# Kernel optimization log

Measured on AMD Instinct MI355X. Metric: run time of the kernel, lower is better.

Reference implementation:

```python
import jax, jax.numpy as jnp
import numpy as np

E = 1024   # embd_size
H = 16     # head_count
HS = E // H
B = 8
T = 1024   # seq len == input_size
EPS = 1e-5

def _ln(x, g, b):
    m = jnp.mean(x, axis=-1, keepdims=True)
    v = jnp.mean((x - m) ** 2, axis=-1, keepdims=True)
    return (x - m) * jax.lax.rsqrt(v + EPS) * g + b

def setup_inputs() -> dict:
    key = jax.random.key(0)
    ks = jax.random.split(key, 12)
    s_attn = 1.0 / np.sqrt(E)
    s_ff1 = 1.0 / np.sqrt(E)
    s_ff2 = 1.0 / np.sqrt(4 * E)
    return {
        "x": jax.random.normal(ks[0], (B, T, E), dtype=jnp.float32),
        "wq": jax.random.normal(ks[1], (H, E, HS), dtype=jnp.float32) * s_attn,
        "wk": jax.random.normal(ks[2], (H, E, HS), dtype=jnp.float32) * s_attn,
        "wv": jax.random.normal(ks[3], (H, E, HS), dtype=jnp.float32) * s_attn,
        "w_proj": jax.random.normal(ks[4], (E, E), dtype=jnp.float32) * s_attn,
        "b_proj": jnp.zeros((E,), dtype=jnp.float32),
        "w1": jax.random.normal(ks[5], (E, 4 * E), dtype=jnp.float32) * s_ff1,
        "b1": jnp.zeros((4 * E,), dtype=jnp.float32),
        "w2": jax.random.normal(ks[6], (4 * E, E), dtype=jnp.float32) * s_ff2,
        "b2": jnp.zeros((E,), dtype=jnp.float32),
        "g1": jnp.ones((E,), dtype=jnp.float32),
        "be1": jnp.zeros((E,), dtype=jnp.float32),
        "g2": jnp.ones((E,), dtype=jnp.float32),
        "be2": jnp.zeros((E,), dtype=jnp.float32),
    }

def reference(x, wq, wk, wv, w_proj, b_proj, w1, b1, w2, b2, g1, be1, g2, be2):
    Tn = x.shape[1]
    h = _ln(x, g1, be1)
    # per-head projections, batched over heads: [B,T,E] x [H,E,S] -> [B,H,T,S]
    q = jnp.einsum('bte,hes->bhts', h, wq)
    k = jnp.einsum('bte,hes->bhts', h, wk)
    v = jnp.einsum('bte,hes->bhts', h, wv)
    scores = jnp.einsum('bhts,bhus->bhtu', q, k)
    # NOTE: source multiplies by sqrt(T) (x.shape[2] of scores), not 1/sqrt(head_size)
    scores = scores * jnp.float32(Tn) ** 0.5
    causal = jnp.tril(jnp.ones((Tn, Tn), dtype=bool))
    scores = jnp.where(causal, scores, -jnp.inf)
    attn = jax.nn.softmax(scores, axis=-1)
    out = jnp.einsum('bhtu,bhus->bhts', attn, v)           # [B,H,T,S]
    out = out.transpose(0, 2, 1, 3).reshape(x.shape[0], Tn, E)  # concat heads
    out = out @ w_proj + b_proj
    x = x + out
    f = _ln(x, g2, be2)
    f = jax.nn.relu(f @ w1 + b1) @ w2 + b2
    return x + f
```

## Files before the change

kernel.cpp:

```cpp
#include <hip/hip_runtime.h>


typedef unsigned short u16;
typedef __attribute__((ext_vector_type(8))) short  bfx8;
typedef __attribute__((ext_vector_type(4))) float  f32x4;
typedef __attribute__((ext_vector_type(4))) unsigned short u16v4;

#define MFMA16 __builtin_amdgcn_mfma_f32_16x16x32_bf16

__device__ __forceinline__ u16 f2bf(float f) {
    union { float f; unsigned u; } c; c.f = f;
    unsigned r = c.u + 0x7fffu + ((c.u >> 16) & 1u);
    return (u16)(r >> 16);
}
__device__ __forceinline__ float bf2f(u16 b) {
    union { unsigned u; float f; } c; c.u = ((unsigned)b) << 16; return c.f;
}
__device__ __forceinline__ float exp2_fast(float x) {
    float r; asm("v_exp_f32 %0, %1" : "=v"(r) : "v"(x)); return r;
}

__device__ __forceinline__ void gl_lds16(const void* g, void* l) {
    void* gg = (void*)g;
    __builtin_amdgcn_global_load_lds(
        (__attribute__((address_space(1))) void*)gg,
        (__attribute__((address_space(3))) void*)l,
        16, 0, 0);
}

__global__ __launch_bounds__(256)
void transpose_split(const float* __restrict__ src, u16* __restrict__ dhi,
                     u16* __restrict__ dlo, int C, int OS,
                     size_t inBS, size_t outBS)
{
    __shared__ float t[64][65];
    const int tid = threadIdx.x;
    const float* s = src + (size_t)blockIdx.z * inBS
                   + ((size_t)blockIdx.y * 64) * C + (size_t)blockIdx.x * 64;
    const size_t obase = (size_t)blockIdx.z * outBS
                       + ((size_t)blockIdx.x * 64) * OS + (size_t)blockIdx.y * 64;
    {
        const int r = tid >> 2, c4 = (tid & 3) * 16;
#pragma unroll
        for (int k = 0; k < 4; ++k) {
            float4 f = *(const float4*)(s + (size_t)r * C + c4 + k * 4);
            t[r][c4 + k*4 + 0] = f.x; t[r][c4 + k*4 + 1] = f.y;
            t[r][c4 + k*4 + 2] = f.z; t[r][c4 + k*4 + 3] = f.w;
        }
    }
    __syncthreads();
    {
        const int c = tid >> 2, r4 = (tid & 3) * 16;
        bfx8 h0, h1, l0, l1;
#pragma unroll
        for (int k = 0; k < 8; ++k) {
            float v0 = t[r4 + k][c];
            float v1 = t[r4 + 8 + k][c];
            u16 a = f2bf(v0), b = f2bf(v1);
            h0[k] = (short)a; h1[k] = (short)b;
            l0[k] = (short)f2bf(v0 - bf2f(a));
            l1[k] = (short)f2bf(v1 - bf2f(b));
        }
        u16* d = dhi + obase + (size_t)c * OS + r4;
        *(bfx8*)d = h0; *(bfx8*)(d + 8) = h1;
        if (dlo) {
            u16* d2 = dlo + obase + (size_t)c * OS + r4;
            *(bfx8*)d2 = l0; *(bfx8*)(d2 + 8) = l1;
        }
    }
}

__global__ __launch_bounds__(256)
void transpose_v(const u16* __restrict__ v, u16* __restrict__ vT)
{
    const int ut = blockIdx.x, h = blockIdx.y, b = blockIdx.z;
    __shared__ u16 t[64][72];
    const int tid = threadIdx.x;
    {
        const int u = tid >> 2, s4 = (tid & 3) * 16;
        const u16* src = v + ((size_t)(b * 1024 + ut * 64 + u)) * 1024 + h * 64 + s4;
        bfx8 a = *(const bfx8*)src;
        bfx8 c = *(const bfx8*)(src + 8);
#pragma unroll
        for (int k = 0; k < 8; ++k) { t[u][s4 + k] = (u16)a[k]; t[u][s4 + 8 + k] = (u16)c[k]; }
    }
    __syncthreads();
    {
        const int s = tid >> 2, u4 = (tid & 3) * 16;
        bfx8 o0, o1;
#pragma unroll
        for (int k = 0; k < 8; ++k) { o0[k] = (short)t[u4 + k][s]; o1[k] = (short)t[u4 + 8 + k][s]; }
        u16* dst = vT + ((size_t)((b * 16 + h) * 64 + s)) * 1024 + ut * 64 + u4;
        *(bfx8*)dst = o0; *(bfx8*)(dst + 8) = o1;
    }
}

__global__ __launch_bounds__(256)
void ln_split(const float* __restrict__ x, const float* __restrict__ g,
              const float* __restrict__ be, u16* __restrict__ hhi,
              u16* __restrict__ hlo)
{
    const int row = blockIdx.x;
    const int tid = threadIdx.x;
    const float4 v = ((const float4*)(x + (size_t)row * 1024))[tid];
    float s  = v.x + v.y + v.z + v.w;
    float s2 = v.x*v.x + v.y*v.y + v.z*v.z + v.w*v.w;
#pragma unroll
    for (int m = 32; m >= 1; m >>= 1) {
        s  += __shfl_xor(s,  m, 64);
        s2 += __shfl_xor(s2, m, 64);
    }
    __shared__ float rs[4], rq[4];
    if ((tid & 63) == 0) { rs[tid >> 6] = s; rq[tid >> 6] = s2; }
    __syncthreads();
    s  = rs[0] + rs[1] + rs[2] + rs[3];
    s2 = rq[0] + rq[1] + rq[2] + rq[3];
    const float mean = s * (1.0f / 1024.0f);
    const float var  = s2 * (1.0f / 1024.0f) - mean * mean;
    const float inv  = rsqrtf(var + 1e-5f);
    const int col0 = tid * 4;
    float hv[4];
    hv[0] = (v.x - mean) * inv * g[col0+0] + be[col0+0];
    hv[1] = (v.y - mean) * inv * g[col0+1] + be[col0+1];
    hv[2] = (v.z - mean) * inv * g[col0+2] + be[col0+2];
    hv[3] = (v.w - mean) * inv * g[col0+3] + be[col0+3];
    u16v4 hb, lb;
#pragma unroll
    for (int k = 0; k < 4; ++k) {
        u16 a = f2bf(hv[k]);
        hb[k] = a;
        lb[k] = f2bf(hv[k] - bf2f(a));
    }
    *(u16v4*)(hhi + (size_t)row * 1024 + col0) = hb;
    if (hlo) *(u16v4*)(hlo + (size_t)row * 1024 + col0) = lb;
}

#define BM 128
#define BN 128
#define BKT 32

template<int FLAGS>
__global__ __launch_bounds__(256, 2)
void gemm_bt(const u16* __restrict__ A, const u16* __restrict__ Bt,
             void* __restrict__ Cout, const float* __restrict__ bias,
             const float* __restrict__ res, int M, int N, int K)
{
    __shared__ u16 As[BM * BKT];
    __shared__ u16 Bs[BN * BKT];
    const int tid  = threadIdx.x;
    const int lane = tid & 63, wave = tid >> 6;
    const int wr = wave >> 1, wc = wave & 1;
    const int li = lane & 15, lg = lane >> 4;
    const size_t m0 = (size_t)blockIdx.y * BM;
    const size_t n0 = (size_t)blockIdx.x * BN;
    f32x4 acc[4][4] = {};

    const int slot0 = tid, slot1 = tid + 256;
    const int r0 = slot0 >> 2, kc0 = (slot0 & 3) * 8;
    const int r1 = slot1 >> 2, kc1 = (slot1 & 3) * 8;

    for (int kt = 0; kt < K; kt += BKT) {
        __syncthreads();
        gl_lds16(A  + (m0 + r0) * K + kt + kc0, As + slot0 * 8);
        gl_lds16(Bt + (n0 + r0) * K + kt + kc0, Bs + slot0 * 8);
        gl_lds16(A  + (m0 + r1) * K + kt + kc1, As + slot1 * 8);
        gl_lds16(Bt + (n0 + r1) * K + kt + kc1, Bs + slot1 * 8);
        __syncthreads();
        bfx8 af[4], bfr[4];
#pragma unroll
        for (int i = 0; i < 4; ++i)
            af[i] = *(const bfx8*)&As[(wr * 64 + i * 16 + li) * BKT + lg * 8];
#pragma unroll
        for (int j = 0; j < 4; ++j)
            bfr[j] = *(const bfx8*)&Bs[(wc * 64 + j * 16 + li) * BKT + lg * 8];
#pragma unroll
        for (int i = 0; i < 4; ++i)
#pragma unroll
            for (int j = 0; j < 4; ++j)
                acc[i][j] = MFMA16(af[i], bfr[j], acc[i][j], 0, 0, 0);
    }

    float* Cf = (float*)Cout;
    u16*   Cb = (u16*)Cout;
#pragma unroll
    for (int i = 0; i < 4; ++i)
#pragma unroll
        for (int j = 0; j < 4; ++j)
#pragma unroll
            for (int r = 0; r < 4; ++r) {
                const size_t row = m0 + wr * 64 + i * 16 + lg * 4 + r;
                const size_t col = n0 + wc * 64 + j * 16 + li;
                float v = acc[i][j][r];
                if (FLAGS & 1) v += bias[col];
                if (FLAGS & 2) v = fmaxf(v, 0.0f);
                if (FLAGS & 4) v += res[row * (size_t)N + col];
                if (FLAGS & 8) Cf[row * (size_t)N + col] = v;
                else           Cb[row * (size_t)N + col] = f2bf(v);
            }
}

template<int EPI, int SPLIT3>
__global__ __launch_bounds__(512, 2)
void gemm8(const u16* __restrict__ A, const u16* __restrict__ Al,
           const u16* __restrict__ Bt, const u16* __restrict__ Bl,
           u16* __restrict__ C, u16* __restrict__ Clo,
           const float* __restrict__ bias,
           int M, int N, int K, int NBX)
{
    __shared__ u16 Asl[2][2][128 * 64];
    __shared__ u16 Bsl[2][2][128 * 64];
    const int tid = threadIdx.x;
    const int lane = tid & 63, wave = tid >> 6;
    const int wr = wave >> 2, wc = wave & 3;
    const int li = lane & 15, lg = lane >> 4;

    const int bid = blockIdx.x;
    const int nwg = gridDim.x;
    const int cpx = nwg >> 3;
    const int swz = (bid & 7) * cpx + (bid >> 3);
    const int bx = swz % NBX, by = swz / NBX;
    const size_t m0 = (size_t)by * 256, n0 = (size_t)bx * 256;

    char* ldsA = (char*)&Asl[0][0][0];
    char* ldsB = (char*)&Bsl[0][0][0];

    const int KT = K >> 6;

    auto stageA = [&](int j, int h) {
        const u16* src = A;
        int jj = j;
        if (SPLIT3) {
            src = (j < 2 * KT) ? A : Al;
            jj = (j < KT) ? j : ((j < 2 * KT) ? j - KT : j - 2 * KT);
        }
#pragma unroll
        for (int site = 0; site < 2; ++site) {
            const int s = tid + site * 512;
            const int r = s >> 3;
            const int cb = ((s & 7) << 4) ^ ((r & 7) << 4);
            gl_lds16((const char*)(src + (m0 + h * 128 + r) * (size_t)K + (size_t)jj * 64) + cb,
                     ldsA + ((j & 1) * 2 + h) * 16384 + s * 16);
        }
    };
    auto stageB = [&](int j, int h) {
        const u16* src = Bt;
        int jj = j;
        if (SPLIT3) {
            src = (j < KT) ? Bt : ((j < 2 * KT) ? Bl : Bt);
            jj = (j < KT) ? j : ((j < 2 * KT) ? j - KT : j - 2 * KT);
        }
#pragma unroll
        for (int site = 0; site < 2; ++site) {
            const int s = tid + site * 512;
            const int r = s >> 3;
            const int cb = ((s & 7) << 4) ^ ((r & 7) << 4);
            gl_lds16((const char*)(src + (n0 + h * 128 + r) * (size_t)K + (size_t)jj * 64) + cb,
                     ldsB + ((j & 1) * 2 + h) * 16384 + s * 16);
        }
    };

    const int lsw = (li & 7) << 4;
    const int aHalfBase = wr * 16384;
    const int bHalfBase = (wc >> 1) * 16384;
    const int bRow0 = (wc & 1) * 64;

    f32x4 acc[8][4] = {};
    const int NT = SPLIT3 ? 3 * KT : KT;
    const int NI = NT >> 1;

    stageA(0, 0); stageA(0, 1); stageB(0, 0); stageB(0, 1);
    stageB(1, 0); stageB(1, 1);
    asm volatile("s_waitcnt vmcnt(0)" ::: "memory");
    __builtin_amdgcn_sched_barrier(0);
    __builtin_amdgcn_s_barrier();
    __builtin_amdgcn_sched_barrier(0);

    for (int t = 0; t < NI; ++t) {
        const bool more = (t + 1 < NI);
#pragma unroll
        for (int half = 0; half < 2; ++half) {
            const int buf = half;
            const int abase = buf * 32768 + aHalfBase;
            const int bbase = buf * 32768 + bHalfBase;
            bfx8 bfr[4][2];
#pragma unroll
            for (int q = 0; q < 4; ++q) {
                if (q == 0) {
#pragma unroll
                    for (int nf = 0; nf < 4; ++nf)
#pragma unroll
                        for (int ks = 0; ks < 2; ++ks)
                            bfr[nf][ks] = *(const bfx8*)(ldsB + bbase
                                + (bRow0 + nf * 16 + li) * 128
                                + ((ks * 64 + lg * 16) ^ lsw));
                }
                bfx8 afr[2][2];
#pragma unroll
                for (int m = 0; m < 2; ++m)
#pragma unroll
                    for (int ks = 0; ks < 2; ++ks)
                        afr[m][ks] = *(const bfx8*)(ldsA + abase
                            + ((2 * q + m) * 16 + li) * 128
                            + ((ks * 64 + lg * 16) ^ lsw));

                if (half == 0) {
                    if (q == 0) stageA(2 * t + 1, 0);
                    else if (q == 1) stageA(2 * t + 1, 1);
                    else if (q == 2) { if (more) stageB(2 * t + 2, 0); }
                    else             { if (more) stageB(2 * t + 2, 1); }
                } else {
                    if (q == 0)      { if (more) stageA(2 * t + 2, 0); }
                    else if (q == 1) { if (more) stageA(2 * t + 2, 1); }
                    else if (q == 2) { if (more) stageB(2 * t + 3, 0); }
                    else             { if (more) stageB(2 * t + 3, 1); }
                }

                __builtin_amdgcn_sched_barrier(0);
                __builtin_amdgcn_s_barrier();
                asm volatile("s_waitcnt lgkmcnt(0)" ::: "memory");
                __builtin_amdgcn_sched_barrier(0);
                __builtin_amdgcn_s_setprio(1);
#pragma unroll
                for (int ks = 0; ks < 2; ++ks)
#pragma unroll
                    for (int m = 0; m < 2; ++m)
#pragma unroll
                        for (int nf = 0; nf < 4; ++nf)
                            acc[2 * q + m][nf] = MFMA16(afr[m][ks], bfr[nf][ks],
                                                        acc[2 * q + m][nf], 0, 0, 0);
                __builtin_amdgcn_s_setprio(0);
                __builtin_amdgcn_sched_barrier(0);
                if (q == 3) {
                    if (half == 0) {
                        if (more) { asm volatile("s_waitcnt vmcnt(4)" ::: "memory"); }
                        else      { asm volatile("s_waitcnt vmcnt(0)" ::: "memory"); }
                    } else if (more) {
                        asm volatile("s_waitcnt vmcnt(4)" ::: "memory");
                    }
                    __builtin_amdgcn_sched_barrier(0);
                }
                __builtin_amdgcn_s_barrier();
                __builtin_amdgcn_sched_barrier(0);
            }
        }
    }

#pragma unroll
    for (int i = 0; i < 8; ++i)
#pragma unroll
        for (int nf = 0; nf < 4; ++nf)
#pragma unroll
            for (int r = 0; r < 4; ++r) {
                const size_t row = m0 + wr * 128 + i * 16 + lg * 4 + r;
                const size_t col = n0 + wc * 64 + nf * 16 + li;
                if (EPI == 0) {
                    float v = acc[i][nf][r] + bias[col];
                    v = fmaxf(v, 0.0f);
                    C[row * (size_t)N + col] = f2bf(v);
                } else {
                    const float v = acc[i][nf][r];
                    const u16 hi = f2bf(v);
                    C[row * (size_t)N + col]   = hi;
                    Clo[row * (size_t)N + col] = f2bf(v - bf2f(hi));
                }
            }
}

#define QKS 2048

__global__ __launch_bounds__(256, 3)
void attn(const u16* __restrict__ qkhi, const u16* __restrict__ qklo,
          const u16* __restrict__ vt, u16* __restrict__ ao)
{
    const int id  = blockIdx.x;
    const int swz = (id & 7) * 256 + (id >> 3);
    const int qt  = 15 - (swz & 15);
    const int h   = (swz >> 4) & 15;
    const int b   = swz >> 8;

    const int tid = threadIdx.x;
    const int wave = tid >> 6, lane = tid & 63;
    const int li = lane & 15, lg = lane >> 4;

    __shared__ u16 KsHi[2][4096];
    __shared__ u16 KsLo[2][4096];
    __shared__ u16 Pl[64 * 64];

    const size_t qrow = (size_t)b * 1024 + qt * 64 + wave * 16 + li;
    const size_t qoff = qrow * QKS + h * 64 + lg * 8;
    const bfx8 qh0 = *(const bfx8*)(qkhi + qoff);
    const bfx8 qh1 = *(const bfx8*)(qkhi + qoff + 32);
    const bfx8 ql0 = *(const bfx8*)(qklo + qoff);
    const bfx8 ql1 = *(const bfx8*)(qklo + qoff + 32);

    bfx8 onesf;
#pragma unroll
    for (int k = 0; k < 8; ++k) onesf[k] = (short)0x3F80;

    f32x4 O[4] = {};
    f32x4 O5 = {0.f, 0.f, 0.f, 0.f};
    float mrow[4] = {-3e38f, -3e38f, -3e38f, -3e38f};

    const u16* kh_base = qkhi + ((size_t)b * 1024) * QKS + 1024 + h * 64;
    const u16* kl_base = qklo + ((size_t)b * 1024) * QKS + 1024 + h * 64;
    const u16* v_base  = vt + ((size_t)(b * 16 + h) * 64) * 1024;

    auto stageK = [&](int kt, int bufIdx) {
#pragma unroll
        for (int site = 0; site < 2; ++site) {
            const int s = tid + site * 256;
            const int r = s >> 3;
            const int cb = (((s & 7) << 4) ^ ((r & 7) << 4));
            const size_t go = ((size_t)(kt * 64 + r)) * QKS;
            gl_lds16((const char*)(kh_base + go) + cb, (char*)&KsHi[bufIdx][0] + s * 16);
            gl_lds16((const char*)(kl_base + go) + cb, (char*)&KsLo[bufIdx][0] + s * 16);
        }
    };

    const int rswz = (li & 7) << 4;
    char* pband = (char*)&Pl[0] + wave * 2048;

    stageK(0, 0);

    for (int kt = 0; kt <= qt; ++kt) {
        const int cur = kt & 1;

        bfx8 vld[2][4];
#pragma unroll
        for (int nf = 0; nf < 4; ++nf) {
            const u16* vr = v_base + ((size_t)(nf * 16 + li)) * 1024 + kt * 64 + lg * 8;
            vld[0][nf] = *(const bfx8*)vr;
            vld[1][nf] = *(const bfx8*)(vr + 32);
        }

        if (kt < qt) {
            stageK(kt + 1, cur ^ 1);
            asm volatile("s_waitcnt vmcnt(12)" ::: "memory");
        } else {
            asm volatile("s_waitcnt vmcnt(8)" ::: "memory");
        }
        __builtin_amdgcn_sched_barrier(0);
        __builtin_amdgcn_s_barrier();
        __builtin_amdgcn_sched_barrier(0);

        float sv[4][4];
        const char* khc = (const char*)&KsHi[cur][0];
        const char* klc = (const char*)&KsLo[cur][0];
#pragma unroll
        for (int nf = 0; nf < 4; ++nf) {
            const int rb = (nf * 16 + li) * 128;
            bfx8 kh0v = *(const bfx8*)(khc + rb + (((lg * 16) + 0 ) ^ rswz));
            bfx8 kh1v = *(const bfx8*)(khc + rb + (((lg * 16) + 64) ^ rswz));
            bfx8 kl0v = *(const bfx8*)(klc + rb + (((lg * 16) + 0 ) ^ rswz));
            bfx8 kl1v = *(const bfx8*)(klc + rb + (((lg * 16) + 64) ^ rswz));
            f32x4 a = {0.f, 0.f, 0.f, 0.f};
            a = MFMA16(qh0, kh0v, a, 0, 0, 0);
            a = MFMA16(qh1, kh1v, a, 0, 0, 0);
            a = MFMA16(qh0, kl0v, a, 0, 0, 0);
            a = MFMA16(qh1, kl1v, a, 0, 0, 0);
            a = MFMA16(ql0, kh0v, a, 0, 0, 0);
            a = MFMA16(ql1, kh1v, a, 0, 0, 0);
#pragma unroll
            for (int r = 0; r < 4; ++r) sv[nf][r] = a[r];
        }

        asm volatile("s_waitcnt lgkmcnt(0)" ::: "memory");
        __builtin_amdgcn_sched_barrier(0);
        __builtin_amdgcn_s_barrier();
        __builtin_amdgcn_sched_barrier(0);

        const float SC = 46.16624130844683f;
        float pmax[4] = {-3e38f, -3e38f, -3e38f, -3e38f};
        if (kt == qt) {
            const int rowg = qt * 64 + wave * 16 + lg * 4;
            const int colg = kt * 64 + li;
#pragma unroll
            for (int nf = 0; nf < 4; ++nf)
#pragma unroll
                for (int r = 0; r < 4; ++r) {
                    float x2 = sv[nf][r] * SC;
                    if (colg + nf * 16 > rowg + r) x2 = -3e38f;
                    sv[nf][r] = x2;
                    pmax[r] = fmaxf(pmax[r], x2);
                }
        } else {
#pragma unroll
            for (int nf = 0; nf < 4; ++nf)
#pragma unroll
                for (int r = 0; r < 4; ++r) {
                    const float x2 = sv[nf][r] * SC;
                    sv[nf][r] = x2;
                    pmax[r] = fmaxf(pmax[r], x2);
                }
        }
#pragma unroll
        for (int msk = 1; msk < 16; msk <<= 1)
#pragma unroll
            for (int r = 0; r < 4; ++r)
                pmax[r] = fmaxf(pmax[r], __shfl_xor(pmax[r], msk, 64));

        const bool grow = !__all((pmax[0] - mrow[0] <= 11.5416f) &&
                                 (pmax[1] - mrow[1] <= 11.5416f) &&
                                 (pmax[2] - mrow[2] <= 11.5416f) &&
                                 (pmax[3] - mrow[3] <= 11.5416f));
        if (grow) {
            float alr[4];
#pragma unroll
            for (int r = 0; r < 4; ++r) {
                const float mnew = fmaxf(mrow[r], pmax[r]);
                alr[r] = exp2_fast(mrow[r] - mnew);
                mrow[r] = mnew;
            }
#pragma unroll
            for (int nf = 0; nf < 4; ++nf)
#pragma unroll
                for (int r = 0; r < 4; ++r)
                    O[nf][r] *= alr[r];
#pragma unroll
            for (int r = 0; r < 4; ++r)
                O5[r] *= alr[r];
        }

#pragma unroll
        for (int nf = 0; nf < 4; ++nf)
#pragma unroll
            for (int r = 0; r < 4; ++r) {
                const int prow = lg * 4 + r;
                const int pb = prow * 128 + ((((nf * 16 + li) * 2)) ^ ((prow & 7) << 4));
                *(u16*)(pband + pb) = f2bf(exp2_fast(sv[nf][r] - mrow[r]));
            }

#pragma unroll
        for (int ku = 0; ku < 2; ++ku) {
            bfx8 pf = *(const bfx8*)(pband + li * 128
                                     + ((ku * 64 + lg * 16) ^ ((li & 7) << 4)));
#pragma unroll
            for (int nf = 0; nf < 4; ++nf)
                O[nf] = MFMA16(pf, vld[ku][nf], O[nf], 0, 0, 0);
            O5 = MFMA16(pf, onesf, O5, 0, 0, 0);
        }
    }

    float invl[4];
#pragma unroll
    for (int r = 0; r < 4; ++r) invl[r] = 1.0f / O5[r];
    const size_t orow = (size_t)b * 1024 + qt * 64 + wave * 16 + lg * 4;
#pragma unroll
    for (int nf = 0; nf < 4; ++nf)
#pragma unroll
        for (int r = 0; r < 4; ++r)
            ao[(orow + r) * 1024 + h * 64 + nf * 16 + li] = f2bf(O[nf][r] * invl[r]);
}

extern "C" void kernel_launch(void* const* d_in, const int* in_sizes, int n_in,
                              void* d_out, int out_size, void* d_ws, size_t ws_size,
                              hipStream_t stream)
{
    (void)in_sizes; (void)n_in; (void)out_size; (void)ws_size;
    const float* x      = (const float*)d_in[0];
    const float* wq     = (const float*)d_in[1];
    const float* wk     = (const float*)d_in[2];
    const float* wv     = (const float*)d_in[3];
    const float* w_proj = (const float*)d_in[4];
    const float* b_proj = (const float*)d_in[5];
    const float* w1     = (const float*)d_in[6];
    const float* b1     = (const float*)d_in[7];
    const float* w2     = (const float*)d_in[8];
    const float* b2     = (const float*)d_in[9];
    const float* g1     = (const float*)d_in[10];
    const float* be1    = (const float*)d_in[11];
    const float* g2     = (const float*)d_in[12];
    const float* be2    = (const float*)d_in[13];
    float* out = (float*)d_out;

    const size_t MB = (size_t)1024 * 1024;
    char* wsp = (char*)d_ws;
    u16* h_hi  = (u16*)(wsp + 0 * MB);
    u16* h_lo  = (u16*)(wsp + 16 * MB);
    u16* qk_hi = (u16*)(wsp + 32 * MB);
    u16* qk_lo = (u16*)(wsp + 64 * MB);
    u16* v_b   = (u16*)(wsp + 96 * MB);
    u16* vtr   = (u16*)(wsp + 112 * MB);
    float* y   = (float*)(wsp + 128 * MB);
    u16* wqkT_hi = (u16*)(wsp + 160 * MB);
    u16* wqkT_lo = (u16*)(wsp + 164 * MB);
    u16* wvT     = (u16*)(wsp + 168 * MB);
    u16* wpT     = (u16*)(wsp + 170 * MB);
    u16* w1T     = (u16*)(wsp + 172 * MB);
    u16* w2T     = (u16*)(wsp + 180 * MB);
    u16* f2  = h_hi;
    u16* ao  = h_lo;
    u16* act = qk_hi;

    dim3 blk(256);

    transpose_split<<<dim3(1, 16, 16), blk, 0, stream>>>(wq, wqkT_hi, wqkT_lo, 64, 1024, (size_t)65536, (size_t)65536);
    transpose_split<<<dim3(1, 16, 16), blk, 0, stream>>>(wk, wqkT_hi + (size_t)1024 * 1024, wqkT_lo + (size_t)1024 * 1024, 64, 1024, (size_t)65536, (size_t)65536);
    transpose_split<<<dim3(1, 16, 16), blk, 0, stream>>>(wv, wvT, nullptr, 64, 1024, (size_t)65536, (size_t)65536);
    transpose_split<<<dim3(16, 16, 1), blk, 0, stream>>>(w_proj, wpT, nullptr, 1024, 1024, 0, 0);
    transpose_split<<<dim3(64, 16, 1), blk, 0, stream>>>(w1, w1T, nullptr, 4096, 1024, 0, 0);
    transpose_split<<<dim3(16, 64, 1), blk, 0, stream>>>(w2, w2T, nullptr, 1024, 4096, 0, 0);

    ln_split<<<8192, blk, 0, stream>>>(x, g1, be1, h_hi, h_lo);

    gemm8<1, 1><<<dim3(256), dim3(512), 0, stream>>>(h_hi, h_lo, wqkT_hi, wqkT_lo,
                                                     qk_hi, qk_lo, nullptr,
                                                     8192, 2048, 1024, 8);
    gemm_bt<0><<<dim3(8, 64), blk, 0, stream>>>(h_hi, wvT, v_b, nullptr, nullptr, 8192, 1024, 1024);
    transpose_v<<<dim3(16, 16, 8), blk, 0, stream>>>(v_b, vtr);

    attn<<<dim3(2048), blk, 0, stream>>>(qk_hi, qk_lo, vtr, ao);

    gemm_bt<1 | 4 | 8><<<dim3(8, 64), blk, 0, stream>>>(ao, wpT, y, b_proj, x, 8192, 1024, 1024);

    ln_split<<<8192, blk, 0, stream>>>(y, g2, be2, f2, nullptr);

    gemm8<0, 0><<<dim3(512), dim3(512), 0, stream>>>(f2, nullptr, w1T, nullptr,
                                                     act, nullptr, b1,
                                                     8192, 4096, 1024, 16);
    gemm_bt<1 | 4 | 8><<<dim3(8, 64), blk, 0, stream>>>(act, w2T, out, b2, y, 8192, 1024, 4096);
}
```

Baseline: 522.6 us.

## Compute V transposed directly via swapped GEMM and load K-lo from global

The V projection is now computed as W_v^T times h^T, so the GEMM writes V already transposed in a [H*64, B*1024] layout. This removes the separate transpose_v kernel and its round trip through memory. In attention, the low half of K is no longer staged through LDS; each lane loads it straight from global memory into registers, which halves the K staging LDS and may raise occupancy. The cost is more uncoalesced global loads per tile, and the wait counts were retuned to match.

```diff
diff --git a/kernel.cpp b/kernel.cpp
--- a/kernel.cpp
+++ b/kernel.cpp
@@ -67,31 +67,6 @@
             u16* d2 = dlo + obase + (size_t)c * OS + r4;
             *(bfx8*)d2 = l0; *(bfx8*)(d2 + 8) = l1;
         }
-    }
-}
-
-__global__ __launch_bounds__(256)
-void transpose_v(const u16* __restrict__ v, u16* __restrict__ vT)
-{
-    const int ut = blockIdx.x, h = blockIdx.y, b = blockIdx.z;
-    __shared__ u16 t[64][72];
-    const int tid = threadIdx.x;
-    {
-        const int u = tid >> 2, s4 = (tid & 3) * 16;
-        const u16* src = v + ((size_t)(b * 1024 + ut * 64 + u)) * 1024 + h * 64 + s4;
-        bfx8 a = *(const bfx8*)src;
-        bfx8 c = *(const bfx8*)(src + 8);
-#pragma unroll
-        for (int k = 0; k < 8; ++k) { t[u][s4 + k] = (u16)a[k]; t[u][s4 + 8 + k] = (u16)c[k]; }
-    }
-    __syncthreads();
-    {
-        const int s = tid >> 2, u4 = (tid & 3) * 16;
-        bfx8 o0, o1;
-#pragma unroll
-        for (int k = 0; k < 8; ++k) { o0[k] = (short)t[u4 + k][s]; o1[k] = (short)t[u4 + 8 + k][s]; }
-        u16* dst = vT + ((size_t)((b * 16 + h) * 64 + s)) * 1024 + ut * 64 + u4;
-        *(bfx8*)dst = o0; *(bfx8*)(dst + 8) = o1;
     }
 }
 
@@ -383,7 +358,6 @@
     const int li = lane & 15, lg = lane >> 4;
 
     __shared__ u16 KsHi[2][4096];
-    __shared__ u16 KsLo[2][4096];
     __shared__ u16 Pl[64 * 64];
 
     const size_t qrow = (size_t)b * 1024 + qt * 64 + wave * 16 + li;
@@ -403,7 +377,7 @@
 
     const u16* kh_base = qkhi + ((size_t)b * 1024) * QKS + 1024 + h * 64;
     const u16* kl_base = qklo + ((size_t)b * 1024) * QKS + 1024 + h * 64;
-    const u16* v_base  = vt + ((size_t)(b * 16 + h) * 64) * 1024;
+    const u16* v_base  = vt + ((size_t)(h * 64)) * 8192 + (size_t)b * 1024;
 
     auto stageK = [&](int kt, int bufIdx) {
 #pragma unroll
@@ -413,7 +387,6 @@
             const int cb = (((s & 7) << 4) ^ ((r & 7) << 4));
             const size_t go = ((size_t)(kt * 64 + r)) * QKS;
             gl_lds16((const char*)(kh_base + go) + cb, (char*)&KsHi[bufIdx][0] + s * 16);
-            gl_lds16((const char*)(kl_base + go) + cb, (char*)&KsLo[bufIdx][0] + s * 16);
         }
     };
 
@@ -428,16 +401,23 @@
         bfx8 vld[2][4];
 #pragma unroll
         for (int nf = 0; nf < 4; ++nf) {
-            const u16* vr = v_base + ((size_t)(nf * 16 + li)) * 1024 + kt * 64 + lg * 8;
+            const u16* vr = v_base + ((size_t)(nf * 16 + li)) * 8192 + kt * 64 + lg * 8;
             vld[0][nf] = *(const bfx8*)vr;
             vld[1][nf] = *(const bfx8*)(vr + 32);
         }
+        bfx8 kld[2][4];
+#pragma unroll
+        for (int nf = 0; nf < 4; ++nf) {
+            const u16* kr = kl_base + ((size_t)(kt * 64 + nf * 16 + li)) * QKS + lg * 8;
+            kld[0][nf] = *(const bfx8*)kr;
+            kld[1][nf] = *(const bfx8*)(kr + 32);
+        }
 
         if (kt < qt) {
             stageK(kt + 1, cur ^ 1);
-            asm volatile("s_waitcnt vmcnt(12)" ::: "memory");
+            asm volatile("s_waitcnt vmcnt(18)" ::: "memory");
         } else {
-            asm volatile("s_waitcnt vmcnt(8)" ::: "memory");
+            asm volatile("s_waitcnt vmcnt(16)" ::: "memory");
         }
         __builtin_amdgcn_sched_barrier(0);
         __builtin_amdgcn_s_barrier();
@@ -445,19 +425,16 @@
 
         float sv[4][4];
         const char* khc = (const char*)&KsHi[cur][0];
-        const char* klc = (const char*)&KsLo[cur][0];
 #pragma unroll
         for (int nf = 0; nf < 4; ++nf) {
             const int rb = (nf * 16 + li) * 128;
             bfx8 kh0v = *(const bfx8*)(khc + rb + (((lg * 16) + 0 ) ^ rswz));
             bfx8 kh1v = *(const bfx8*)(khc + rb + (((lg * 16) + 64) ^ rswz));
-            bfx8 kl0v = *(const bfx8*)(klc + rb + (((lg * 16) + 0 ) ^ rswz));
-            bfx8 kl1v = *(const bfx8*)(klc + rb + (((lg * 16) + 64) ^ rswz));
             f32x4 a = {0.f, 0.f, 0.f, 0.f};
             a = MFMA16(qh0, kh0v, a, 0, 0, 0);
             a = MFMA16(qh1, kh1v, a, 0, 0, 0);
-            a = MFMA16(qh0, kl0v, a, 0, 0, 0);
-            a = MFMA16(qh1, kl1v, a, 0, 0, 0);
+            a = MFMA16(qh0, kld[0][nf], a, 0, 0, 0);
+            a = MFMA16(qh1, kld[1][nf], a, 0, 0, 0);
             a = MFMA16(ql0, kh0v, a, 0, 0, 0);
             a = MFMA16(ql1, kh1v, a, 0, 0, 0);
 #pragma unroll
@@ -579,7 +556,6 @@
     u16* h_lo  = (u16*)(wsp + 16 * MB);
     u16* qk_hi = (u16*)(wsp + 32 * MB);
     u16* qk_lo = (u16*)(wsp + 64 * MB);
-    u16* v_b   = (u16*)(wsp + 96 * MB);
     u16* vtr   = (u16*)(wsp + 112 * MB);
     float* y   = (float*)(wsp + 128 * MB);
     u16* wqkT_hi = (u16*)(wsp + 160 * MB);
@@ -606,8 +582,7 @@
     gemm8<1, 1><<<dim3(256), dim3(512), 0, stream>>>(h_hi, h_lo, wqkT_hi, wqkT_lo,
                                                      qk_hi, qk_lo, nullptr,
                                                      8192, 2048, 1024, 8);
-    gemm_bt<0><<<dim3(8, 64), blk, 0, stream>>>(h_hi, wvT, v_b, nullptr, nullptr, 8192, 1024, 1024);
-    transpose_v<<<dim3(16, 16, 8), blk, 0, stream>>>(v_b, vtr);
+    gemm_bt<0><<<dim3(64, 8), blk, 0, stream>>>(wvT, h_hi, vtr, nullptr, nullptr, 1024, 8192, 1024);
 
     attn<<<dim3(2048), blk, 0, stream>>>(qk_hi, qk_lo, vtr, ao);
 
```

Measured after the change: 585.4 us. +12.0%, slower.
